# Kernel optimization log

Hardware: AMD Instinct MI355X
Metric: run time of the kernel (lower is better)

The kernel has to match this reference:

```python
import jax, jax.numpy as jnp
import numpy as np
from jax import lax

B, S, C, L = 256, 30, 62, 169   # batch, timesteps, channels(nodes), data_seg
OG, OH = 64, 64                 # out_gcn, out_gru
K1, K2, K3 = 64, 32, 14         # depthwise kernel sizes (169-63-31-13 = 62 = C)


def setup_inputs() -> dict:
    key = jax.random.key(0)
    ks = jax.random.split(key, 26)
    def n(k, shape, s=0.05):
        return jax.random.normal(k, shape, dtype=jnp.float32) * s
    inp = {
        "x": jax.random.normal(ks[0], (B, S, C, L), dtype=jnp.float32),
        "adj": jax.random.normal(ks[1], (C, C), dtype=jnp.float32),
        # depthwise-separable conv 1 (kernel 64)
        "dw1_w": n(ks[2], (C, 1, K1)), "dw1_b": n(ks[3], (C,)),
        "pw1_w": n(ks[4], (C, C, 1)), "pw1_b": n(ks[5], (C,)),
        # depthwise-separable conv 2 (kernel 32)
        "dw2_w": n(ks[6], (C, 1, K2)), "dw2_b": n(ks[7], (C,)),
        "pw2_w": n(ks[8], (C, C, 1)), "pw2_b": n(ks[9], (C,)),
        # depthwise-separable conv 3 (kernel 14)
        "dw3_w": n(ks[10], (C, 1, K3)), "dw3_b": n(ks[11], (C,)),
        "pw3_w": n(ks[12], (C, C, 1)), "pw3_b": n(ks[13], (C,)),
        # GraphConvolution(data_seg, out_gcn): support = x @ W; out = adj @ support + b
        "gcn_w": n(ks[14], (L, OG)), "gcn_b": n(ks[15], (OG,)),
        # GRU-style gate Linears (out_gcn+out_gru -> out_gru), torch layout (out, in)
        "Wr_w": n(ks[16], (OH, OG + OH)), "Wr_b": n(ks[17], (OH,)),
        "Wu_w": n(ks[18], (OH, OG + OH)), "Wu_b": n(ks[19], (OH,)),
        "Wc_w": n(ks[20], (OH, OG + OH)), "Wc_b": n(ks[21], (OH,)),
        # extra learned gate biases b_r/b_u/b_c (init zeros in torch)
        "b_r": jnp.zeros((OH,), jnp.float32),
        "b_u": jnp.zeros((OH,), jnp.float32),
        "b_c": jnp.zeros((OH,), jnp.float32),
    }
    return inp


def _dsconv(x, dw, dwb, pw, pwb):
    # x: (b, c, l); depthwise (groups=c, valid padding) then pointwise 1x1
    dn = ("NCH", "OIH", "NCH")
    y = lax.conv_general_dilated(x, dw, (1,), "VALID", dimension_numbers=dn,
                                 feature_group_count=x.shape[1]) + dwb[None, :, None]
    y = lax.conv_general_dilated(y, pw, (1,), "VALID", dimension_numbers=dn) + pwb[None, :, None]
    return y


def reference(x, adj, dw1_w, dw1_b, pw1_w, pw1_b, dw2_w, dw2_b, pw2_w, pw2_b,
              dw3_w, dw3_b, pw3_w, pw3_b, gcn_w, gcn_b,
              Wr_w, Wr_b, Wu_w, Wu_b, Wc_w, Wc_b, b_r, b_u, b_c):
    b, s, c, l = x.shape
    oh = b_r.shape[0]

    def step(h, xt):            # h: (b*c, oh), xt: (b, c, l)
        d = _dsconv(xt, dw1_w, dw1_b, pw1_w, pw1_b)
        d = _dsconv(d, dw2_w, dw2_b, pw2_w, pw2_b)
        d = _dsconv(d, dw3_w, dw3_b, pw3_w, pw3_b)      # (b, c, c)
        adj_t = jax.nn.sigmoid(d + adj)                  # adaptive adjacency
        support = jnp.einsum("bcl,lf->bcf", xt, gcn_w)
        g = jnp.einsum("bij,bjf->bif", adj_t, support) + gcn_b  # (b, c, og)
        gf = g.reshape(b * c, -1)
        cat = jnp.concatenate([gf, h], axis=-1)
        r = jax.nn.sigmoid(cat @ Wr_w.T + Wr_b + b_r)
        u = jax.nn.sigmoid(cat @ Wu_w.T + Wu_b + b_u)
        cc = jnp.tanh(jnp.concatenate([gf, r * h], axis=-1) @ Wc_w.T + Wc_b + b_c)
        h_new = u * h + (1.0 - u) * cc
        return h_new, None

    h0 = jnp.zeros((b * c, oh), x.dtype)
    xs = jnp.swapaxes(x, 0, 1)          # (s, b, c, l)
    h_last, _ = lax.scan(step, h0, xs)
    return h_last.reshape(b, c, oh)[:, -1, :]   # (b, out_gru)
```

## Files before the change

### kernel.cpp

```cpp
#include <hip/hip_runtime.h>
#include <math.h>

#define BB 256
#define SS 30
#define CC 62
#define LL 169
#define OG 64
#define OH 64
#define KK1 64
#define KK2 32
#define KK3 14
#define FLEN 108

typedef __attribute__((ext_vector_type(8))) short s16x8;
typedef __attribute__((ext_vector_type(4))) float f32x4;

__device__ __forceinline__ unsigned short f2bf(float f) {
    unsigned u = __float_as_uint(f);
    u += 0x7fffu + ((u >> 16) & 1u);
    return (unsigned short)(u >> 16);
}
__device__ __forceinline__ float bflo(unsigned v) { return __uint_as_float(v << 16); }
__device__ __forceinline__ float bfhi(unsigned v) { return __uint_as_float(v & 0xffff0000u); }

__global__ __launch_bounds__(1024) void k_setup1(
        const float* __restrict__ dw1, const float* __restrict__ dw1b,
        const float* __restrict__ pw1, const float* __restrict__ pw1b,
        const float* __restrict__ dw2, const float* __restrict__ dw2b,
        const float* __restrict__ pw2, const float* __restrict__ pw2b,
        const float* __restrict__ dw3, const float* __restrict__ dw3b,
        const float* __restrict__ pw3, const float* __restrict__ pw3b,
        const float* __restrict__ Wr, const float* __restrict__ Wrb, const float* __restrict__ br,
        const float* __restrict__ Wu, const float* __restrict__ Wub, const float* __restrict__ bu,
        const float* __restrict__ Wc, const float* __restrict__ Wcb, const float* __restrict__ bc,
        float* __restrict__ Bmg, float* __restrict__ WtAll,
        float* __restrict__ bias192, float* __restrict__ beff) {
    __shared__ float g23[CC * KK3];
    __shared__ float Am[CC * 45];
    __shared__ float by2[CC], vals[CC];
    int tid = threadIdx.x;

    for (int idx = tid; idx < OG * 192; idx += 1024) {
        int i = idx / 192, q = idx - i * 192;
        int gate = q >> 6, f = q & 63;
        const float* W = gate == 0 ? Wr : (gate == 1 ? Wu : Wc);
        WtAll[idx] = W[f * (OG + OH) + i];
    }
    if (tid < 192) {
        int gate = tid >> 6, f = tid & 63;
        const float* Wb = gate == 0 ? Wrb : (gate == 1 ? Wub : Wcb);
        const float* bb = gate == 0 ? br  : (gate == 1 ? bu  : bc);
        bias192[tid] = Wb[f] + bb[f];
    }
    for (int idx = tid; idx < CC * KK3; idx += 1024) {
        int c1 = idx / KK3, k3 = idx - c1 * KK3;
        float s = 0.f;
        for (int c2 = 0; c2 < CC; ++c2)
            s += pw3[61 * CC + c2] * pw2[c2 * CC + c1] * dw3[c2 * KK3 + k3];
        g23[idx] = s;
    }
    if (tid < CC) {
        int c1 = tid;
        float bz1 = pw1b[c1];
        for (int c0 = 0; c0 < CC; ++c0) bz1 += pw1[c1 * CC + c0] * dw1b[c0];
        float s2 = 0.f;
        for (int k = 0; k < KK2; ++k) s2 += dw2[c1 * KK2 + k];
        by2[c1] = dw2b[c1] + bz1 * s2;
    }
    __syncthreads();
    if (tid < CC) {
        int c2 = tid;
        float bz2 = pw2b[c2];
        for (int c1 = 0; c1 < CC; ++c1) bz2 += pw2[c2 * CC + c1] * by2[c1];
        float s3 = 0.f;
        for (int k = 0; k < KK3; ++k) s3 += dw3[c2 * KK3 + k];
        vals[c2] = pw3[61 * CC + c2] * (dw3b[c2] + bz2 * s3);
    }
    for (int idx = tid; idx < CC * 45; idx += 1024) {
        int c1 = idx / 45, m = idx - c1 * 45;
        int k2lo = max(0, m - (KK3 - 1));
        int k2hi = min(KK2 - 1, m);
        float s = 0.f;
        for (int k2 = k2lo; k2 <= k2hi; ++k2)
            s += dw2[c1 * KK2 + k2] * g23[c1 * KK3 + (m - k2)];
        Am[idx] = s;
    }
    __syncthreads();
    if (tid == 0) {
        float s = pw3b[61];
        for (int c2 = 0; c2 < CC; ++c2) s += vals[c2];
        *beff = s;
    }
    for (int idx = tid; idx < CC * 45; idx += 1024) {
        int c0 = idx / 45, m = idx - c0 * 45;
        float s = 0.f;
        for (int c1 = 0; c1 < CC; ++c1) s += pw1[c1 * CC + c0] * Am[c1 * 45 + m];
        Bmg[idx] = s;
    }
}

__global__ __launch_bounds__(128) void k_setupF(
        const float* __restrict__ Bmg, const float* __restrict__ dw1,
        unsigned short* __restrict__ Ftb) {
    __shared__ float Bl[45];
    int c0 = blockIdx.x;
    int o = threadIdx.x;
    if (c0 < CC && o < 45) Bl[o] = Bmg[c0 * 45 + o];
    __syncthreads();
    if (o >= 112) return;
    float s = 0.f;
    if (c0 < CC && o < FLEN) {
        int mlo = max(0, o - (KK1 - 1));
        int mhi = min(44, o);
        for (int m = mlo; m <= mhi; ++m)
            s += Bl[m] * dw1[c0 * KK1 + (o - m)];
    }
    Ftb[o * 64 + c0] = f2bf(s);
}

#define STG_ISSUE(i, s) do {                                                   \
    const float* pA = xg + 338 * cpa[i] + l0a[i];                              \
    const float* pB = pA + 169;                                                \
    asm volatile("global_load_dwordx2 %0, %1, off" : "=v"(A0[s]) : "v"(pA));   \
    asm volatile("global_load_dwordx2 %0, %1, off" : "=v"(A1[s]) : "v"(pA + 2));\
    asm volatile("global_load_dwordx2 %0, %1, off" : "=v"(B0[s]) : "v"(pB));   \
    asm volatile("global_load_dwordx2 %0, %1, off" : "=v"(B1[s]) : "v"(pB + 2));\
} while (0)

#define STG_CONSUME(i, s, VM) do {                                             \
    asm volatile("s_waitcnt vmcnt(" VM ")"                                     \
        : "+v"(A0[s]), "+v"(A1[s]), "+v"(B0[s]), "+v"(B1[s]));                 \
    unsigned d0, d1, d2, d3;                                                   \
    asm("v_cvt_pk_bf16_f32 %0, %1, %2" : "=v"(d0)                             \
        : "v"(__uint_as_float(A0[s].x)), "v"(__uint_as_float(B0[s].x)));       \
    asm("v_cvt_pk_bf16_f32 %0, %1, %2" : "=v"(d1)                             \
        : "v"(__uint_as_float(A0[s].y)), "v"(__uint_as_float(B0[s].y)));       \
    asm("v_cvt_pk_bf16_f32 %0, %1, %2" : "=v"(d2)                             \
        : "v"(__uint_as_float(A1[s].x)), "v"(__uint_as_float(B1[s].x)));       \
    asm("v_cvt_pk_bf16_f32 %0, %1, %2" : "=v"(d3)                             \
        : "v"(__uint_as_float(A1[s].y)), "v"(__uint_as_float(B1[s].y)));       \
    int l0 = l0a[i], cp = cpa[i];                                              \
    xTu[((l0 + 0) * 32 + cp) ^ (((l0 + 0) & 7) << 2)] = d0;                    \
    xTu[((l0 + 1) * 32 + cp) ^ (((l0 + 1) & 7) << 2)] = d1;                    \
    xTu[((l0 + 2) * 32 + cp) ^ (((l0 + 2) & 7) << 2)] = d2;                    \
    xTu[((l0 + 3) * 32 + cp) ^ (((l0 + 3) & 7) << 2)] = d3;                    \
} while (0)

__global__ __launch_bounds__(256, 3) void k_main(
        const float* __restrict__ x, const float* __restrict__ adj,
        const unsigned short* __restrict__ Ftb, const float* __restrict__ beff_p,
        float* __restrict__ wxb) {
    __shared__ __align__(16) unsigned short xT[176 * 64];
    __shared__ float dacc[4][64];
    __shared__ __align__(16) unsigned adjbf[32];
    int bt = blockIdx.x;
    int tid = threadIdx.x;
    int lane = tid & 63, wid = tid >> 6;
    int col = lane & 15, rb4 = lane >> 4;
    unsigned* xTu = (unsigned*)xT;
    const float* xg = x + (size_t)bt * (CC * LL);

    float be = *beff_p;
    float2 arow2 = make_float2(0.f, 0.f);
    if (tid < 31) arow2 = *(const float2*)(adj + 61 * CC + 2 * tid);
    const unsigned short* ap0 = Ftb + ((wid * 16 + col) * 64 + rb4 * 8);
    s16x8 pa0 = *(const s16x8*)ap0;
    s16x8 pa1 = *(const s16x8*)(ap0 + 32);
    int mt2c = wid + 4 < 7 ? wid + 4 : 6;
    const unsigned short* ap1 = Ftb + ((mt2c * 16 + col) * 64 + rb4 * 8);
    s16x8 pb0 = *(const s16x8*)ap1;
    s16x8 pb1 = *(const s16x8*)(ap1 + 32);
    __builtin_amdgcn_sched_barrier(0);

    uint2 A0[3], A1[3], B0[3], B1[3];
    int l0a[6], cpa[6];
    #pragma unroll
    for (int i = 0; i < 6; ++i) {
        int w = tid + i * 256; if (w > 1332) w = 1332;
        int lg = w / 31; cpa[i] = w - lg * 31;
        l0a[i] = (lg < 42) ? 4 * lg : 165;
    }
    STG_ISSUE(0, 0); STG_ISSUE(1, 1); STG_ISSUE(2, 2);
    for (int i = tid; i < 169; i += 256) xTu[(i * 32 + 31) ^ ((i & 7) << 2)] = 0;
    for (int i = tid; i < 224; i += 256) {
        int r = 169 + (i >> 5), dd = i & 31;
        xTu[(r * 32 + dd) ^ ((r & 7) << 2)] = 0;
    }
    ((float*)dacc)[tid] = 0.f;

    STG_CONSUME(0, 0, "8"); STG_ISSUE(3, 0);
    STG_CONSUME(1, 1, "8"); STG_ISSUE(4, 1);
    STG_CONSUME(2, 2, "8"); STG_ISSUE(5, 2);
    STG_CONSUME(3, 0, "8");
    STG_CONSUME(4, 1, "4");
    STG_CONSUME(5, 2, "0");
    __syncthreads();

    f32x4 zacc[5];
    #pragma unroll
    for (int d = 0; d < 5; ++d) zacc[d] = (f32x4){0.f, 0.f, 0.f, 0.f};
    int kb = rb4 * 16;
    int xr = (lane & 7) << 4;
    #pragma unroll
    for (int h = 0; h < 2; ++h) {
        int mt = wid + 4 * h;
        if (mt < 7) {
            s16x8 a0 = h == 0 ? pa0 : pb0;
            s16x8 a1 = h == 0 ? pa1 : pb1;
            #pragma unroll
            for (int d = 0; d < 5; ++d) {
                int nt = mt + d;
                int bbyte = ((nt * 16 + col) * 128 + kb) ^ xr;
                s16x8 b0 = *(const s16x8*)((const char*)xT + bbyte);
                s16x8 b1 = *(const s16x8*)((const char*)xT + (bbyte ^ 64));
                zacc[d] = __builtin_amdgcn_mfma_f32_16x16x32_bf16(a0, b0, zacc[d], 0, 0, 0);
                zacc[d] = __builtin_amdgcn_mfma_f32_16x16x32_bf16(a1, b1, zacc[d], 0, 0, 0);
            }
        }
    }
    int jc = col - rb4 * 4;
    #pragma unroll
    for (int d = 0; d < 5; ++d) {
        #pragma unroll
        for (int r = 0; r < 4; ++r) {
            int j = 16 * d + jc - r;
            if ((unsigned)j < 62u) atomicAdd(&dacc[rb4][j], zacc[d][r]);
        }
    }
    __syncthreads();

    if (tid < 32) {
        unsigned pk = 0;
        if (tid < 31) {
            int j0 = 2 * tid;
            float2 g0 = *(const float2*)(&dacc[0][j0]);
            float2 g1 = *(const float2*)(&dacc[1][j0]);
            float2 g2 = *(const float2*)(&dacc[2][j0]);
            float2 g3 = *(const float2*)(&dacc[3][j0]);
            float dv0 = (g0.x + g1.x) + (g2.x + g3.x) + be + arow2.x;
            float dv1 = (g0.y + g1.y) + (g2.y + g3.y) + be + arow2.y;
            float s0 = 1.f / (1.f + __expf(-dv0));
            float s1 = 1.f / (1.f + __expf(-dv1));
            asm("v_cvt_pk_bf16_f32 %0, %1, %2" : "=v"(pk) : "v"(s0), "v"(s1));
        }
        adjbf[tid] = pk;
    }
    __syncthreads();

    {
        s16x8 wa0 = *(const s16x8*)(adjbf + rb4 * 4);
        s16x8 wa1 = *(const s16x8*)(adjbf + 16 + rb4 * 4);
        #pragma unroll
        for (int q = 0; q < 3; ++q) {
            int nt = wid + 4 * q;
            if (nt < 11) {
                int bbyte = ((nt * 16 + col) * 128 + kb) ^ xr;
                s16x8 b0 = *(const s16x8*)((const char*)xT + bbyte);
                s16x8 b1 = *(const s16x8*)((const char*)xT + (bbyte ^ 64));
                f32x4 wacc = {0.f, 0.f, 0.f, 0.f};
                wacc = __builtin_amdgcn_mfma_f32_16x16x32_bf16(wa0, b0, wacc, 0, 0, 0);
                wacc = __builtin_amdgcn_mfma_f32_16x16x32_bf16(wa1, b1, wacc, 0, 0, 0);
                if (rb4 == 0) wxb[(size_t)bt * 176 + nt * 16 + col] = wacc[0];
            }
        }
    }
}

__global__ __launch_bounds__(256) void k_gg(
        const float* __restrict__ wxb, const float* __restrict__ gcnw,
        const float* __restrict__ gcnb, const float* __restrict__ WtAll,
        const float* __restrict__ bias192, float* __restrict__ gates) {
    __shared__ float wxl[8 * 176];
    __shared__ float Gl[8 * 64];
    int bt0 = blockIdx.x * 8;
    int tid = threadIdx.x;
    const float* src = wxb + (size_t)bt0 * 176;
    for (int i = tid; i < 8 * 176; i += 256) wxl[i] = src[i];
    __syncthreads();
    #pragma unroll
    for (int rep = 0; rep < 2; ++rep) {
        int i = rep * 256 + tid;
        int bl = i >> 6, f = i & 63;
        float s = gcnb[f];
        const float* wr = wxl + bl * 176;
        #pragma unroll 13
        for (int l = 0; l < LL; ++l) s += wr[l] * gcnw[l * OG + f];
        Gl[i] = s;
    }
    __syncthreads();
    float* gout = gates + (size_t)bt0 * 192;
    #pragma unroll
    for (int rep = 0; rep < 6; ++rep) {
        int i = rep * 256 + tid;
        int bl = i / 192, q = i - bl * 192;
        const float* gr = Gl + bl * 64;
        float s = bias192[q];
        #pragma unroll 16
        for (int k = 0; k < OG; ++k) s += gr[k] * WtAll[k * 192 + q];
        gout[i] = s;
    }
}

__global__ __launch_bounds__(256) void k_scan(
        const float* __restrict__ gates,
        const float* __restrict__ Wr, const float* __restrict__ Wu, const float* __restrict__ Wc,
        float* __restrict__ out) {
    __shared__ float hl[OH], rhl[OH];
    int b = blockIdx.x;
    int tid = threadIdx.x;
    int f = tid >> 2, q = tid & 3;
    float wr[16], wu[16], wc[16];
    #pragma unroll
    for (int i = 0; i < 16; ++i) {
        int col = OG + q * 16 + i;
        wr[i] = Wr[f * (OG + OH) + col];
        wu[i] = Wu[f * (OG + OH) + col];
        wc[i] = Wc[f * (OG + OH) + col];
    }
    float h = 0.f;
    if (tid < OH) hl[tid] = 0.f;
    __syncthreads();
    for (int t = 0; t < SS; ++t) {
        const float* gp = gates + ((size_t)b * SS + t) * 192;
        float gr = gp[f];
        float gu = gp[64 + f];
        float gc = gp[128 + f];
        float rv = 0.f, uv = 0.f;
        #pragma unroll
        for (int i = 0; i < 16; ++i) {
            float hv = hl[q * 16 + i];
            rv += wr[i] * hv;
            uv += wu[i] * hv;
        }
        rv += __shfl_xor(rv, 1); rv += __shfl_xor(rv, 2);
        uv += __shfl_xor(uv, 1); uv += __shfl_xor(uv, 2);
        float r = 1.f / (1.f + __expf(-(rv + gr)));
        float u = 1.f / (1.f + __expf(-(uv + gu)));
        if (q == 0) rhl[f] = r * h;
        __syncthreads();
        float cv = 0.f;
        #pragma unroll
        for (int i = 0; i < 16; ++i) cv += wc[i] * rhl[q * 16 + i];
        cv += __shfl_xor(cv, 1); cv += __shfl_xor(cv, 2);
        float cc = tanhf(cv + gc);
        if (q == 0) {
            h = u * h + (1.f - u) * cc;
            hl[f] = h;
        }
        __syncthreads();
    }
    if (q == 0) out[b * OH + f] = h;
}

extern "C" void kernel_launch(void* const* d_in, const int* in_sizes, int n_in,
                              void* d_out, int out_size, void* d_ws, size_t ws_size,
                              hipStream_t stream) {
    const float* x    = (const float*)d_in[0];
    const float* adj  = (const float*)d_in[1];
    const float* dw1w = (const float*)d_in[2];
    const float* dw1b = (const float*)d_in[3];
    const float* pw1w = (const float*)d_in[4];
    const float* pw1b = (const float*)d_in[5];
    const float* dw2w = (const float*)d_in[6];
    const float* dw2b = (const float*)d_in[7];
    const float* pw2w = (const float*)d_in[8];
    const float* pw2b = (const float*)d_in[9];
    const float* dw3w = (const float*)d_in[10];
    const float* dw3b = (const float*)d_in[11];
    const float* pw3w = (const float*)d_in[12];
    const float* pw3b = (const float*)d_in[13];
    const float* gcnw = (const float*)d_in[14];
    const float* gcnb = (const float*)d_in[15];
    const float* Wrw  = (const float*)d_in[16];
    const float* Wrb  = (const float*)d_in[17];
    const float* Wuw  = (const float*)d_in[18];
    const float* Wub  = (const float*)d_in[19];
    const float* Wcw  = (const float*)d_in[20];
    const float* Wcb  = (const float*)d_in[21];
    const float* br   = (const float*)d_in[22];
    const float* bu   = (const float*)d_in[23];
    const float* bc   = (const float*)d_in[24];
    float* out = (float*)d_out;

    char* ws = (char*)d_ws;
    unsigned short* Ftb = (unsigned short*)(ws + 0);
    float* WtAll        = (float*)(ws + 14336);
    float* bias192      = (float*)(ws + 63488);
    float* beff         = (float*)(ws + 64256);
    float* Bmg          = (float*)(ws + 64320);
    float* wxb          = (float*)(ws + 76800);
    float* gates        = (float*)(ws + 5483520);
    (void)ws_size; (void)in_sizes; (void)n_in; (void)out_size;

    k_setup1<<<1, 1024, 0, stream>>>(dw1w, dw1b, pw1w, pw1b, dw2w, dw2b, pw2w, pw2b,
                                     dw3w, dw3b, pw3w, pw3b,
                                     Wrw, Wrb, br, Wuw, Wub, bu, Wcw, Wcb, bc,
                                     Bmg, WtAll, bias192, beff);
    k_setupF<<<64, 128, 0, stream>>>(Bmg, dw1w, Ftb);
    k_main<<<BB * SS, 256, 0, stream>>>(x, adj, Ftb, beff, wxb);
    k_gg<<<BB * SS / 8, 256, 0, stream>>>(wxb, gcnw, gcnb, WtAll, bias192, gates);
    k_scan<<<BB, 256, 0, stream>>>(gates, Wrw, Wuw, Wcw, out);
}
```

Baseline: 280.9 us.

## Fuse GCN and gate projection into main kernel; stage x via contiguous LDS chunks

Removes the separate k_gg kernel and the wxb round trip through global memory. Each k_main block now computes the GCN output and the 192 gate pre-activations itself from an LDS copy of its wx row. The x load is also restructured: coalesced contiguous chunks of 8 channels go through a double-buffered LDS staging buffer and are then transposed into the bf16 xT layout. This adds extra LDS (about 11 KB), many block barriers in the load phase, and per-block gcnw/WtAll reads that were previously amortised over 8 rows, which may hurt occupancy under launch_bounds(256,3).

```diff
diff --git a/kernel.cpp b/kernel.cpp
--- a/kernel.cpp
+++ b/kernel.cpp
@@ -20,8 +20,6 @@
     u += 0x7fffu + ((u >> 16) & 1u);
     return (unsigned short)(u >> 16);
 }
-__device__ __forceinline__ float bflo(unsigned v) { return __uint_as_float(v << 16); }
-__device__ __forceinline__ float bfhi(unsigned v) { return __uint_as_float(v & 0xffff0000u); }
 
 __global__ __launch_bounds__(1024) void k_setup1(
         const float* __restrict__ dw1, const float* __restrict__ dw1b,
@@ -118,41 +116,68 @@
     Ftb[o * 64 + c0] = f2bf(s);
 }
 
-#define STG_ISSUE(i, s) do {                                                   \
-    const float* pA = xg + 338 * cpa[i] + l0a[i];                              \
-    const float* pB = pA + 169;                                                \
-    asm volatile("global_load_dwordx2 %0, %1, off" : "=v"(A0[s]) : "v"(pA));   \
-    asm volatile("global_load_dwordx2 %0, %1, off" : "=v"(A1[s]) : "v"(pA + 2));\
-    asm volatile("global_load_dwordx2 %0, %1, off" : "=v"(B0[s]) : "v"(pB));   \
-    asm volatile("global_load_dwordx2 %0, %1, off" : "=v"(B1[s]) : "v"(pB + 2));\
+#define CH_ISSUE(ch) do {                                                          \
+    const int nd2 = ((ch) < 7) ? 676 : 507;                                        \
+    const float* cb = xg + 1352 * (ch);                                            \
+    _Pragma("unroll")                                                              \
+    for (int j = 0; j < 3; ++j) {                                                  \
+        int pos = tid + j * 256; if (pos > nd2 - 1) pos = nd2 - 1;                 \
+        asm volatile("global_load_dwordx2 %0, %1, off"                             \
+                     : "=v"(SL[(ch) & 1][j]) : "v"(cb + 2 * pos));                 \
+    }                                                                              \
 } while (0)
 
-#define STG_CONSUME(i, s, VM) do {                                             \
-    asm volatile("s_waitcnt vmcnt(" VM ")"                                     \
-        : "+v"(A0[s]), "+v"(A1[s]), "+v"(B0[s]), "+v"(B1[s]));                 \
-    unsigned d0, d1, d2, d3;                                                   \
-    asm("v_cvt_pk_bf16_f32 %0, %1, %2" : "=v"(d0)                             \
-        : "v"(__uint_as_float(A0[s].x)), "v"(__uint_as_float(B0[s].x)));       \
-    asm("v_cvt_pk_bf16_f32 %0, %1, %2" : "=v"(d1)                             \
-        : "v"(__uint_as_float(A0[s].y)), "v"(__uint_as_float(B0[s].y)));       \
-    asm("v_cvt_pk_bf16_f32 %0, %1, %2" : "=v"(d2)                             \
-        : "v"(__uint_as_float(A1[s].x)), "v"(__uint_as_float(B1[s].x)));       \
-    asm("v_cvt_pk_bf16_f32 %0, %1, %2" : "=v"(d3)                             \
-        : "v"(__uint_as_float(A1[s].y)), "v"(__uint_as_float(B1[s].y)));       \
-    int l0 = l0a[i], cp = cpa[i];                                              \
-    xTu[((l0 + 0) * 32 + cp) ^ (((l0 + 0) & 7) << 2)] = d0;                    \
-    xTu[((l0 + 1) * 32 + cp) ^ (((l0 + 1) & 7) << 2)] = d1;                    \
-    xTu[((l0 + 2) * 32 + cp) ^ (((l0 + 2) & 7) << 2)] = d2;                    \
-    xTu[((l0 + 3) * 32 + cp) ^ (((l0 + 3) & 7) << 2)] = d3;                    \
+#define CH_CONSUME(ch, VM) do {                                                    \
+    asm volatile("s_waitcnt vmcnt(" VM ")"                                         \
+        : "+v"(SL[(ch) & 1][0]), "+v"(SL[(ch) & 1][1]), "+v"(SL[(ch) & 1][2]));    \
+    {                                                                              \
+        const int nd2 = ((ch) < 7) ? 676 : 507;                                    \
+        uint2* cb2 = (uint2*)chunkbuf[(ch) & 1];                                   \
+        _Pragma("unroll")                                                          \
+        for (int j = 0; j < 3; ++j) {                                              \
+            int pos = tid + j * 256; if (pos > nd2 - 1) pos = nd2 - 1;             \
+            cb2[pos] = SL[(ch) & 1][j];                                            \
+        }                                                                          \
+    }                                                                              \
+    asm volatile("s_waitcnt lgkmcnt(0)" ::: "memory");                             \
+    __builtin_amdgcn_sched_barrier(0);                                             \
+    __builtin_amdgcn_s_barrier();                                                  \
+    {                                                                              \
+        const int ncp = ((ch) < 7) ? 4 : 3;                                        \
+        const unsigned* cb = (const unsigned*)chunkbuf[(ch) & 1];                  \
+        int cpL = tid & 3, lb = tid >> 2;                                          \
+        _Pragma("unroll")                                                          \
+        for (int it = 0; it < 3; ++it) {                                           \
+            int l = lb + 64 * it;                                                  \
+            if (l < LL && cpL < ncp) {                                             \
+                unsigned lo = cb[(2 * cpL) * LL + l];                              \
+                unsigned hi = cb[(2 * cpL + 1) * LL + l];                          \
+                unsigned v;                                                        \
+                asm("v_cvt_pk_bf16_f32 %0, %1, %2" : "=v"(v)                       \
+                    : "v"(__uint_as_float(lo)), "v"(__uint_as_float(hi)));         \
+                int cp = (ch) * 4 + cpL;                                           \
+                xTu[(l * 32 + cp) ^ ((l & 7) << 2)] = v;                           \
+            }                                                                      \
+        }                                                                          \
+    }                                                                              \
+    asm volatile("s_waitcnt lgkmcnt(0)" ::: "memory");                             \
+    __builtin_amdgcn_sched_barrier(0);                                             \
+    __builtin_amdgcn_s_barrier();                                                  \
 } while (0)
 
 __global__ __launch_bounds__(256, 3) void k_main(
         const float* __restrict__ x, const float* __restrict__ adj,
         const unsigned short* __restrict__ Ftb, const float* __restrict__ beff_p,
-        float* __restrict__ wxb) {
+        const float* __restrict__ gcnw, const float* __restrict__ gcnb,
+        const float* __restrict__ WtAll, const float* __restrict__ bias192,
+        float* __restrict__ gates) {
     __shared__ __align__(16) unsigned short xT[176 * 64];
+    __shared__ __align__(16) char chunkbuf[2][5408];
     __shared__ float dacc[4][64];
     __shared__ __align__(16) unsigned adjbf[32];
+    __shared__ float wxl[176];
+    __shared__ float gpart[4][64];
+    __shared__ float Gl[64];
     int bt = blockIdx.x;
     int tid = threadIdx.x;
     int lane = tid & 63, wid = tid >> 6;
@@ -168,19 +193,12 @@
     s16x8 pa1 = *(const s16x8*)(ap0 + 32);
     int mt2c = wid + 4 < 7 ? wid + 4 : 6;
     const unsigned short* ap1 = Ftb + ((mt2c * 16 + col) * 64 + rb4 * 8);
-    s16x8 pb0 = *(const s16x8*)ap1;
+    s16x8 pb0 = *(const s16x8*)(ap1);
     s16x8 pb1 = *(const s16x8*)(ap1 + 32);
     __builtin_amdgcn_sched_barrier(0);
 
-    uint2 A0[3], A1[3], B0[3], B1[3];
-    int l0a[6], cpa[6];
-    #pragma unroll
-    for (int i = 0; i < 6; ++i) {
-        int w = tid + i * 256; if (w > 1332) w = 1332;
-        int lg = w / 31; cpa[i] = w - lg * 31;
-        l0a[i] = (lg < 42) ? 4 * lg : 165;
-    }
-    STG_ISSUE(0, 0); STG_ISSUE(1, 1); STG_ISSUE(2, 2);
+    uint2 SL[2][3];
+    CH_ISSUE(0); CH_ISSUE(1);
     for (int i = tid; i < 169; i += 256) xTu[(i * 32 + 31) ^ ((i & 7) << 2)] = 0;
     for (int i = tid; i < 224; i += 256) {
         int r = 169 + (i >> 5), dd = i & 31;
@@ -188,13 +206,14 @@
     }
     ((float*)dacc)[tid] = 0.f;
 
-    STG_CONSUME(0, 0, "8"); STG_ISSUE(3, 0);
-    STG_CONSUME(1, 1, "8"); STG_ISSUE(4, 1);
-    STG_CONSUME(2, 2, "8"); STG_ISSUE(5, 2);
-    STG_CONSUME(3, 0, "8");
-    STG_CONSUME(4, 1, "4");
-    STG_CONSUME(5, 2, "0");
-    __syncthreads();
+    CH_CONSUME(0, "3"); CH_ISSUE(2);
+    CH_CONSUME(1, "3"); CH_ISSUE(3);
+    CH_CONSUME(2, "3"); CH_ISSUE(4);
+    CH_CONSUME(3, "3"); CH_ISSUE(5);
+    CH_CONSUME(4, "3"); CH_ISSUE(6);
+    CH_CONSUME(5, "3"); CH_ISSUE(7);
+    CH_CONSUME(6, "3");
+    CH_CONSUME(7, "0");
 
     f32x4 zacc[5];
     #pragma unroll
@@ -260,44 +279,28 @@
                 f32x4 wacc = {0.f, 0.f, 0.f, 0.f};
                 wacc = __builtin_amdgcn_mfma_f32_16x16x32_bf16(wa0, b0, wacc, 0, 0, 0);
                 wacc = __builtin_amdgcn_mfma_f32_16x16x32_bf16(wa1, b1, wacc, 0, 0, 0);
-                if (rb4 == 0) wxb[(size_t)bt * 176 + nt * 16 + col] = wacc[0];
+                if (rb4 == 0) wxl[nt * 16 + col] = wacc[0];
             }
         }
     }
-}
-
-__global__ __launch_bounds__(256) void k_gg(
-        const float* __restrict__ wxb, const float* __restrict__ gcnw,
-        const float* __restrict__ gcnb, const float* __restrict__ WtAll,
-        const float* __restrict__ bias192, float* __restrict__ gates) {
-    __shared__ float wxl[8 * 176];
-    __shared__ float Gl[8 * 64];
-    int bt0 = blockIdx.x * 8;
-    int tid = threadIdx.x;
-    const float* src = wxb + (size_t)bt0 * 176;
-    for (int i = tid; i < 8 * 176; i += 256) wxl[i] = src[i];
-    __syncthreads();
-    #pragma unroll
-    for (int rep = 0; rep < 2; ++rep) {
-        int i = rep * 256 + tid;
-        int bl = i >> 6, f = i & 63;
-        float s = gcnb[f];
-        const float* wr = wxl + bl * 176;
-        #pragma unroll 13
-        for (int l = 0; l < LL; ++l) s += wr[l] * gcnw[l * OG + f];
-        Gl[i] = s;
-    }
-    __syncthreads();
-    float* gout = gates + (size_t)bt0 * 192;
-    #pragma unroll
-    for (int rep = 0; rep < 6; ++rep) {
-        int i = rep * 256 + tid;
-        int bl = i / 192, q = i - bl * 192;
-        const float* gr = Gl + bl * 64;
-        float s = bias192[q];
+    __syncthreads();
+
+    {
+        int f = tid & 63, lq = tid >> 6;
+        float s = 0.f;
+        for (int l = lq; l < LL; l += 4) s += wxl[l] * gcnw[l * OG + f];
+        gpart[lq][f] = s;
+    }
+    __syncthreads();
+    if (tid < OG)
+        Gl[tid] = gcnb[tid] + gpart[0][tid] + gpart[1][tid] + gpart[2][tid] + gpart[3][tid];
+    __syncthreads();
+
+    if (tid < 192) {
+        float s = bias192[tid];
         #pragma unroll 16
-        for (int k = 0; k < OG; ++k) s += gr[k] * WtAll[k * 192 + q];
-        gout[i] = s;
+        for (int k = 0; k < OG; ++k) s += Gl[k] * WtAll[k * 192 + tid];
+        gates[(size_t)bt * 192 + tid] = s;
     }
 }
 
@@ -388,8 +391,7 @@
     float* bias192      = (float*)(ws + 63488);
     float* beff         = (float*)(ws + 64256);
     float* Bmg          = (float*)(ws + 64320);
-    float* wxb          = (float*)(ws + 76800);
-    float* gates        = (float*)(ws + 5483520);
+    float* gates        = (float*)(ws + 76800);
     (void)ws_size; (void)in_sizes; (void)n_in; (void)out_size;
 
     k_setup1<<<1, 1024, 0, stream>>>(dw1w, dw1b, pw1w, pw1b, dw2w, dw2b, pw2w, pw2b,
@@ -397,7 +399,7 @@
                                      Wrw, Wrb, br, Wuw, Wub, bu, Wcw, Wcb, bc,
                                      Bmg, WtAll, bias192, beff);
     k_setupF<<<64, 128, 0, stream>>>(Bmg, dw1w, Ftb);
-    k_main<<<BB * SS, 256, 0, stream>>>(x, adj, Ftb, beff, wxb);
-    k_gg<<<BB * SS / 8, 256, 0, stream>>>(wxb, gcnw, gcnb, WtAll, bias192, gates);
+    k_main<<<BB * SS, 256, 0, stream>>>(x, adj, Ftb, beff, gcnw, gcnb,
+                                        WtAll, bias192, gates);
     k_scan<<<BB, 256, 0, stream>>>(gates, Wrw, Wuw, Wcw, out);
 }
```

Measured after the change: 341.1 us. 1.21x slower.

## Make main kernel persistent over tiles with double-buffered prefetch and fused GCN gates

Applied to the files above, without the earlier changes.

The main kernel now handles NT=10 (batch,timestep) tiles per block. The next tile's x is loaded into a second LDS buffer while the current tile's MFMA work runs. The former k_gg GCN/gate projection is fused into the per-tile loop, which removes the wxb round trip through global memory. The two setup kernels are merged into one 64-block kernel that redundantly recomputes Am per block. In exchange, the grid shrinks from 7680 to 768 blocks, LDS use doubles, and each tile now carries several extra barriers plus serial gate GEMV work that may lower occupancy.

```diff
diff --git a/kernel.cpp b/kernel.cpp
--- a/kernel.cpp
+++ b/kernel.cpp
@@ -11,6 +11,7 @@
 #define KK2 32
 #define KK3 14
 #define FLEN 108
+#define NT 10
 
 typedef __attribute__((ext_vector_type(8))) short s16x8;
 typedef __attribute__((ext_vector_type(4))) float f32x4;
@@ -20,10 +21,8 @@
     u += 0x7fffu + ((u >> 16) & 1u);
     return (unsigned short)(u >> 16);
 }
-__device__ __forceinline__ float bflo(unsigned v) { return __uint_as_float(v << 16); }
-__device__ __forceinline__ float bfhi(unsigned v) { return __uint_as_float(v & 0xffff0000u); }
-
-__global__ __launch_bounds__(1024) void k_setup1(
+
+__global__ __launch_bounds__(128) void k_setupAll(
         const float* __restrict__ dw1, const float* __restrict__ dw1b,
         const float* __restrict__ pw1, const float* __restrict__ pw1b,
         const float* __restrict__ dw2, const float* __restrict__ dw2b,
@@ -33,42 +32,44 @@
         const float* __restrict__ Wr, const float* __restrict__ Wrb, const float* __restrict__ br,
         const float* __restrict__ Wu, const float* __restrict__ Wub, const float* __restrict__ bu,
         const float* __restrict__ Wc, const float* __restrict__ Wcb, const float* __restrict__ bc,
-        float* __restrict__ Bmg, float* __restrict__ WtAll,
+        unsigned short* __restrict__ Ftb, float* __restrict__ WtAll,
         float* __restrict__ bias192, float* __restrict__ beff) {
     __shared__ float g23[CC * KK3];
     __shared__ float Am[CC * 45];
+    __shared__ float Bl[45];
     __shared__ float by2[CC], vals[CC];
-    int tid = threadIdx.x;
-
-    for (int idx = tid; idx < OG * 192; idx += 1024) {
-        int i = idx / 192, q = idx - i * 192;
+    int c0 = blockIdx.x, tid = threadIdx.x;
+
+    for (int q = tid; q < 192; q += 128) {
         int gate = q >> 6, f = q & 63;
         const float* W = gate == 0 ? Wr : (gate == 1 ? Wu : Wc);
-        WtAll[idx] = W[f * (OG + OH) + i];
-    }
-    if (tid < 192) {
-        int gate = tid >> 6, f = tid & 63;
-        const float* Wb = gate == 0 ? Wrb : (gate == 1 ? Wub : Wcb);
-        const float* bb = gate == 0 ? br  : (gate == 1 ? bu  : bc);
-        bias192[tid] = Wb[f] + bb[f];
-    }
-    for (int idx = tid; idx < CC * KK3; idx += 1024) {
+        WtAll[c0 * 192 + q] = W[f * (OG + OH) + c0];
+    }
+    if (c0 == 0) {
+        for (int q = tid; q < 192; q += 128) {
+            int gate = q >> 6, f = q & 63;
+            const float* Wb = gate == 0 ? Wrb : (gate == 1 ? Wub : Wcb);
+            const float* bb = gate == 0 ? br  : (gate == 1 ? bu  : bc);
+            bias192[q] = Wb[f] + bb[f];
+        }
+    }
+    if (c0 == 63 && tid < CC) {
+        int c1 = tid;
+        float bz1 = pw1b[c1];
+        for (int cc = 0; cc < CC; ++cc) bz1 += pw1[c1 * CC + cc] * dw1b[cc];
+        float s2 = 0.f;
+        for (int k = 0; k < KK2; ++k) s2 += dw2[c1 * KK2 + k];
+        by2[c1] = dw2b[c1] + bz1 * s2;
+    }
+    for (int idx = tid; idx < CC * KK3; idx += 128) {
         int c1 = idx / KK3, k3 = idx - c1 * KK3;
         float s = 0.f;
         for (int c2 = 0; c2 < CC; ++c2)
             s += pw3[61 * CC + c2] * pw2[c2 * CC + c1] * dw3[c2 * KK3 + k3];
         g23[idx] = s;
     }
-    if (tid < CC) {
-        int c1 = tid;
-        float bz1 = pw1b[c1];
-        for (int c0 = 0; c0 < CC; ++c0) bz1 += pw1[c1 * CC + c0] * dw1b[c0];
-        float s2 = 0.f;
-        for (int k = 0; k < KK2; ++k) s2 += dw2[c1 * KK2 + k];
-        by2[c1] = dw2b[c1] + bz1 * s2;
-    }
     __syncthreads();
-    if (tid < CC) {
+    if (c0 == 63 && tid < CC) {
         int c2 = tid;
         float bz2 = pw2b[c2];
         for (int c1 = 0; c1 < CC; ++c1) bz2 += pw2[c2 * CC + c1] * by2[c1];
@@ -76,7 +77,7 @@
         for (int k = 0; k < KK3; ++k) s3 += dw3[c2 * KK3 + k];
         vals[c2] = pw3[61 * CC + c2] * (dw3b[c2] + bz2 * s3);
     }
-    for (int idx = tid; idx < CC * 45; idx += 1024) {
+    for (int idx = tid; idx < CC * 45; idx += 128) {
         int c1 = idx / 45, m = idx - c1 * 45;
         int k2lo = max(0, m - (KK3 - 1));
         int k2hi = min(KK2 - 1, m);
@@ -86,40 +87,32 @@
         Am[idx] = s;
     }
     __syncthreads();
-    if (tid == 0) {
+    if (c0 == 63 && tid == 0) {
         float s = pw3b[61];
         for (int c2 = 0; c2 < CC; ++c2) s += vals[c2];
         *beff = s;
     }
-    for (int idx = tid; idx < CC * 45; idx += 1024) {
-        int c0 = idx / 45, m = idx - c0 * 45;
+    if (tid < 45 && c0 < CC) {
         float s = 0.f;
-        for (int c1 = 0; c1 < CC; ++c1) s += pw1[c1 * CC + c0] * Am[c1 * 45 + m];
-        Bmg[idx] = s;
+        for (int c1 = 0; c1 < CC; ++c1) s += pw1[c1 * CC + c0] * Am[c1 * 45 + tid];
+        Bl[tid] = s;
+    }
+    __syncthreads();
+    if (tid < 112) {
+        int o = tid;
+        float s = 0.f;
+        if (c0 < CC && o < FLEN) {
+            int mlo = max(0, o - (KK1 - 1));
+            int mhi = min(44, o);
+            for (int m = mlo; m <= mhi; ++m)
+                s += Bl[m] * dw1[c0 * KK1 + (o - m)];
+        }
+        Ftb[o * 64 + c0] = f2bf(s);
     }
 }
 
-__global__ __launch_bounds__(128) void k_setupF(
-        const float* __restrict__ Bmg, const float* __restrict__ dw1,
-        unsigned short* __restrict__ Ftb) {
-    __shared__ float Bl[45];
-    int c0 = blockIdx.x;
-    int o = threadIdx.x;
-    if (c0 < CC && o < 45) Bl[o] = Bmg[c0 * 45 + o];
-    __syncthreads();
-    if (o >= 112) return;
-    float s = 0.f;
-    if (c0 < CC && o < FLEN) {
-        int mlo = max(0, o - (KK1 - 1));
-        int mhi = min(44, o);
-        for (int m = mlo; m <= mhi; ++m)
-            s += Bl[m] * dw1[c0 * KK1 + (o - m)];
-    }
-    Ftb[o * 64 + c0] = f2bf(s);
-}
-
-#define STG_ISSUE(i, s) do {                                                   \
-    const float* pA = xg + 338 * cpa[i] + l0a[i];                              \
+#define SISSUE(tp, i, s) do {                                                  \
+    const float* pA = (tp) + 338 * cpa[i] + l0a[i];                            \
     const float* pB = pA + 169;                                                \
     asm volatile("global_load_dwordx2 %0, %1, off" : "=v"(A0[s]) : "v"(pA));   \
     asm volatile("global_load_dwordx2 %0, %1, off" : "=v"(A1[s]) : "v"(pA + 2));\
@@ -127,7 +120,7 @@
     asm volatile("global_load_dwordx2 %0, %1, off" : "=v"(B1[s]) : "v"(pB + 2));\
 } while (0)
 
-#define STG_CONSUME(i, s, VM) do {                                             \
+#define SCONSUME(i, s, VM, XW) do {                                            \
     asm volatile("s_waitcnt vmcnt(" VM ")"                                     \
         : "+v"(A0[s]), "+v"(A1[s]), "+v"(B0[s]), "+v"(B1[s]));                 \
     unsigned d0, d1, d2, d3;                                                   \
@@ -140,25 +133,29 @@
     asm("v_cvt_pk_bf16_f32 %0, %1, %2" : "=v"(d3)                             \
         : "v"(__uint_as_float(A1[s].y)), "v"(__uint_as_float(B1[s].y)));       \
     int l0 = l0a[i], cp = cpa[i];                                              \
-    xTu[((l0 + 0) * 32 + cp) ^ (((l0 + 0) & 7) << 2)] = d0;                    \
-    xTu[((l0 + 1) * 32 + cp) ^ (((l0 + 1) & 7) << 2)] = d1;                    \
-    xTu[((l0 + 2) * 32 + cp) ^ (((l0 + 2) & 7) << 2)] = d2;                    \
-    xTu[((l0 + 3) * 32 + cp) ^ (((l0 + 3) & 7) << 2)] = d3;                    \
+    (XW)[((l0 + 0) * 32 + cp) ^ (((l0 + 0) & 7) << 2)] = d0;                   \
+    (XW)[((l0 + 1) * 32 + cp) ^ (((l0 + 1) & 7) << 2)] = d1;                   \
+    (XW)[((l0 + 2) * 32 + cp) ^ (((l0 + 2) & 7) << 2)] = d2;                   \
+    (XW)[((l0 + 3) * 32 + cp) ^ (((l0 + 3) & 7) << 2)] = d3;                   \
 } while (0)
 
 __global__ __launch_bounds__(256, 3) void k_main(
         const float* __restrict__ x, const float* __restrict__ adj,
         const unsigned short* __restrict__ Ftb, const float* __restrict__ beff_p,
-        float* __restrict__ wxb) {
-    __shared__ __align__(16) unsigned short xT[176 * 64];
+        const float* __restrict__ gcnw, const float* __restrict__ gcnb,
+        const float* __restrict__ WtAll, const float* __restrict__ bias192,
+        float* __restrict__ gates) {
+    __shared__ __align__(16) unsigned short xT[2][176 * 64];
     __shared__ float dacc[4][64];
     __shared__ __align__(16) unsigned adjbf[32];
-    int bt = blockIdx.x;
+    __shared__ float wxl[176];
+    __shared__ float gpart[4][64];
+    __shared__ float Gl[64];
     int tid = threadIdx.x;
     int lane = tid & 63, wid = tid >> 6;
     int col = lane & 15, rb4 = lane >> 4;
     unsigned* xTu = (unsigned*)xT;
-    const float* xg = x + (size_t)bt * (CC * LL);
+    int btBase = blockIdx.x * NT;
 
     float be = *beff_p;
     float2 arow2 = make_float2(0.f, 0.f);
@@ -168,7 +165,7 @@
     s16x8 pa1 = *(const s16x8*)(ap0 + 32);
     int mt2c = wid + 4 < 7 ? wid + 4 : 6;
     const unsigned short* ap1 = Ftb + ((mt2c * 16 + col) * 64 + rb4 * 8);
-    s16x8 pb0 = *(const s16x8*)ap1;
+    s16x8 pb0 = *(const s16x8*)(ap1);
     s16x8 pb1 = *(const s16x8*)(ap1 + 32);
     __builtin_amdgcn_sched_barrier(0);
 
@@ -180,124 +177,133 @@
         int lg = w / 31; cpa[i] = w - lg * 31;
         l0a[i] = (lg < 42) ? 4 * lg : 165;
     }
-    STG_ISSUE(0, 0); STG_ISSUE(1, 1); STG_ISSUE(2, 2);
-    for (int i = tid; i < 169; i += 256) xTu[(i * 32 + 31) ^ ((i & 7) << 2)] = 0;
-    for (int i = tid; i < 224; i += 256) {
-        int r = 169 + (i >> 5), dd = i & 31;
-        xTu[(r * 32 + dd) ^ ((r & 7) << 2)] = 0;
-    }
-    ((float*)dacc)[tid] = 0.f;
-
-    STG_CONSUME(0, 0, "8"); STG_ISSUE(3, 0);
-    STG_CONSUME(1, 1, "8"); STG_ISSUE(4, 1);
-    STG_CONSUME(2, 2, "8"); STG_ISSUE(5, 2);
-    STG_CONSUME(3, 0, "8");
-    STG_CONSUME(4, 1, "4");
-    STG_CONSUME(5, 2, "0");
-    __syncthreads();
-
-    f32x4 zacc[5];
-    #pragma unroll
-    for (int d = 0; d < 5; ++d) zacc[d] = (f32x4){0.f, 0.f, 0.f, 0.f};
     int kb = rb4 * 16;
     int xr = (lane & 7) << 4;
-    #pragma unroll
-    for (int h = 0; h < 2; ++h) {
-        int mt = wid + 4 * h;
-        if (mt < 7) {
-            s16x8 a0 = h == 0 ? pa0 : pb0;
-            s16x8 a1 = h == 0 ? pa1 : pb1;
+    int jc = col - rb4 * 4;
+
+    {
+        const float* tp0 = x + (size_t)btBase * (CC * LL);
+        SISSUE(tp0, 0, 0); SISSUE(tp0, 1, 1); SISSUE(tp0, 2, 2);
+        for (int b = 0; b < 2; ++b) {
+            unsigned* XW = xTu + b * 5632;
+            for (int i = tid; i < 169; i += 256) XW[(i * 32 + 31) ^ ((i & 7) << 2)] = 0;
+            for (int i = tid; i < 224; i += 256) {
+                int r = 169 + (i >> 5), dd = i & 31;
+                XW[(r * 32 + dd) ^ ((r & 7) << 2)] = 0;
+            }
+        }
+        ((float*)dacc)[tid] = 0.f;
+        unsigned* XW0 = xTu;
+        SCONSUME(0, 0, "8", XW0); SISSUE(tp0, 3, 0);
+        SCONSUME(1, 1, "8", XW0); SISSUE(tp0, 4, 1);
+        SCONSUME(2, 2, "8", XW0); SISSUE(tp0, 5, 2);
+        SCONSUME(3, 0, "8", XW0);
+        SCONSUME(4, 1, "4", XW0);
+        SCONSUME(5, 2, "0", XW0);
+        __syncthreads();
+    }
+
+    for (int t = 0; t < NT; ++t) {
+        int cur = t & 1;
+        const char* xTb = (const char*)xT + cur * 22528;
+        unsigned* XWn = xTu + (cur ^ 1) * 5632;
+        bool more = (t + 1 < NT);
+        const float* tpn = x + (size_t)(btBase + (more ? t + 1 : t)) * (CC * LL);
+        if (more) { SISSUE(tpn, 0, 0); SISSUE(tpn, 1, 1); SISSUE(tpn, 2, 2); }
+
+        f32x4 zacc[5];
+        #pragma unroll
+        for (int d = 0; d < 5; ++d) zacc[d] = (f32x4){0.f, 0.f, 0.f, 0.f};
+        #pragma unroll
+        for (int h = 0; h < 2; ++h) {
+            int mt = wid + 4 * h;
+            if (mt < 7) {
+                s16x8 a0 = h == 0 ? pa0 : pb0;
+                s16x8 a1 = h == 0 ? pa1 : pb1;
+                #pragma unroll
+                for (int d = 0; d < 5; ++d) {
+                    int nt = mt + d;
+                    int bbyte = ((nt * 16 + col) * 128 + kb) ^ xr;
+                    s16x8 b0 = *(const s16x8*)(xTb + bbyte);
+                    s16x8 b1 = *(const s16x8*)(xTb + (bbyte ^ 64));
+                    zacc[d] = __builtin_amdgcn_mfma_f32_16x16x32_bf16(a0, b0, zacc[d], 0, 0, 0);
+                    zacc[d] = __builtin_amdgcn_mfma_f32_16x16x32_bf16(a1, b1, zacc[d], 0, 0, 0);
+                }
+            }
+        }
+        if (more) { SCONSUME(0, 0, "8", XWn); SISSUE(tpn, 3, 0); }
+        #pragma unroll
+        for (int d = 0; d < 5; ++d) {
             #pragma unroll
-            for (int d = 0; d < 5; ++d) {
-                int nt = mt + d;
-                int bbyte = ((nt * 16 + col) * 128 + kb) ^ xr;
-                s16x8 b0 = *(const s16x8*)((const char*)xT + bbyte);
-                s16x8 b1 = *(const s16x8*)((const char*)xT + (bbyte ^ 64));
-                zacc[d] = __builtin_amdgcn_mfma_f32_16x16x32_bf16(a0, b0, zacc[d], 0, 0, 0);
-                zacc[d] = __builtin_amdgcn_mfma_f32_16x16x32_bf16(a1, b1, zacc[d], 0, 0, 0);
+            for (int r = 0; r < 4; ++r) {
+                int j = 16 * d + jc - r;
+                if ((unsigned)j < 62u) atomicAdd(&dacc[rb4][j], zacc[d][r]);
             }
         }
-    }
-    int jc = col - rb4 * 4;
-    #pragma unroll
-    for (int d = 0; d < 5; ++d) {
-        #pragma unroll
-        for (int r = 0; r < 4; ++r) {
-            int j = 16 * d + jc - r;
-            if ((unsigned)j < 62u) atomicAdd(&dacc[rb4][j], zacc[d][r]);
-        }
-    }
-    __syncthreads();
-
-    if (tid < 32) {
-        unsigned pk = 0;
-        if (tid < 31) {
-            int j0 = 2 * tid;
-            float2 g0 = *(const float2*)(&dacc[0][j0]);
-            float2 g1 = *(const float2*)(&dacc[1][j0]);
-            float2 g2 = *(const float2*)(&dacc[2][j0]);
-            float2 g3 = *(const float2*)(&dacc[3][j0]);
-            float dv0 = (g0.x + g1.x) + (g2.x + g3.x) + be + arow2.x;
-            float dv1 = (g0.y + g1.y) + (g2.y + g3.y) + be + arow2.y;
-            float s0 = 1.f / (1.f + __expf(-dv0));
-            float s1 = 1.f / (1.f + __expf(-dv1));
-            asm("v_cvt_pk_bf16_f32 %0, %1, %2" : "=v"(pk) : "v"(s0), "v"(s1));
-        }
-        adjbf[tid] = pk;
-    }
-    __syncthreads();
-
-    {
-        s16x8 wa0 = *(const s16x8*)(adjbf + rb4 * 4);
-        s16x8 wa1 = *(const s16x8*)(adjbf + 16 + rb4 * 4);
-        #pragma unroll
-        for (int q = 0; q < 3; ++q) {
-            int nt = wid + 4 * q;
-            if (nt < 11) {
-                int bbyte = ((nt * 16 + col) * 128 + kb) ^ xr;
-                s16x8 b0 = *(const s16x8*)((const char*)xT + bbyte);
-                s16x8 b1 = *(const s16x8*)((const char*)xT + (bbyte ^ 64));
-                f32x4 wacc = {0.f, 0.f, 0.f, 0.f};
-                wacc = __builtin_amdgcn_mfma_f32_16x16x32_bf16(wa0, b0, wacc, 0, 0, 0);
-                wacc = __builtin_amdgcn_mfma_f32_16x16x32_bf16(wa1, b1, wacc, 0, 0, 0);
-                if (rb4 == 0) wxb[(size_t)bt * 176 + nt * 16 + col] = wacc[0];
+        if (more) { SCONSUME(1, 1, "8", XWn); SISSUE(tpn, 4, 1); }
+        __syncthreads();
+
+        if (more) { SCONSUME(2, 2, "8", XWn); SISSUE(tpn, 5, 2); }
+        if (tid < 32) {
+            unsigned pk = 0;
+            if (tid < 31) {
+                int j0 = 2 * tid;
+                float2 g0 = *(const float2*)(&dacc[0][j0]);
+                float2 g1 = *(const float2*)(&dacc[1][j0]);
+                float2 g2 = *(const float2*)(&dacc[2][j0]);
+                float2 g3 = *(const float2*)(&dacc[3][j0]);
+                float dv0 = (g0.x + g1.x) + (g2.x + g3.x) + be + arow2.x;
+                float dv1 = (g0.y + g1.y) + (g2.y + g3.y) + be + arow2.y;
+                float s0 = 1.f / (1.f + __expf(-dv0));
+                float s1 = 1.f / (1.f + __expf(-dv1));
+                asm("v_cvt_pk_bf16_f32 %0, %1, %2" : "=v"(pk) : "v"(s0), "v"(s1));
             }
-        }
-    }
-}
-
-__global__ __launch_bounds__(256) void k_gg(
-        const float* __restrict__ wxb, const float* __restrict__ gcnw,
-        const float* __restrict__ gcnb, const float* __restrict__ WtAll,
-        const float* __restrict__ bias192, float* __restrict__ gates) {
-    __shared__ float wxl[8 * 176];
-    __shared__ float Gl[8 * 64];
-    int bt0 = blockIdx.x * 8;
-    int tid = threadIdx.x;
-    const float* src = wxb + (size_t)bt0 * 176;
-    for (int i = tid; i < 8 * 176; i += 256) wxl[i] = src[i];
-    __syncthreads();
-    #pragma unroll
-    for (int rep = 0; rep < 2; ++rep) {
-        int i = rep * 256 + tid;
-        int bl = i >> 6, f = i & 63;
-        float s = gcnb[f];
-        const float* wr = wxl + bl * 176;
-        #pragma unroll 13
-        for (int l = 0; l < LL; ++l) s += wr[l] * gcnw[l * OG + f];
-        Gl[i] = s;
-    }
-    __syncthreads();
-    float* gout = gates + (size_t)bt0 * 192;
-    #pragma unroll
-    for (int rep = 0; rep < 6; ++rep) {
-        int i = rep * 256 + tid;
-        int bl = i / 192, q = i - bl * 192;
-        const float* gr = Gl + bl * 64;
-        float s = bias192[q];
-        #pragma unroll 16
-        for (int k = 0; k < OG; ++k) s += gr[k] * WtAll[k * 192 + q];
-        gout[i] = s;
+            adjbf[tid] = pk;
+        }
+        __syncthreads();
+
+        if (more) { SCONSUME(3, 0, "8", XWn); }
+        {
+            s16x8 wa0 = *(const s16x8*)(adjbf + rb4 * 4);
+            s16x8 wa1 = *(const s16x8*)(adjbf + 16 + rb4 * 4);
+            #pragma unroll
+            for (int q = 0; q < 3; ++q) {
+                int nt = wid + 4 * q;
+                if (nt < 11) {
+                    int bbyte = ((nt * 16 + col) * 128 + kb) ^ xr;
+                    s16x8 b0 = *(const s16x8*)(xTb + bbyte);
+                    s16x8 b1 = *(const s16x8*)(xTb + (bbyte ^ 64));
+                    f32x4 wacc = {0.f, 0.f, 0.f, 0.f};
+                    wacc = __builtin_amdgcn_mfma_f32_16x16x32_bf16(wa0, b0, wacc, 0, 0, 0);
+                    wacc = __builtin_amdgcn_mfma_f32_16x16x32_bf16(wa1, b1, wacc, 0, 0, 0);
+                    if (rb4 == 0) wxl[nt * 16 + col] = wacc[0];
+                }
+            }
+        }
+        ((float*)dacc)[tid] = 0.f;
+        __syncthreads();
+
+        if (more) { SCONSUME(4, 1, "4", XWn); }
+        {
+            int f = tid & 63, lq = tid >> 6;
+            float s = 0.f;
+            for (int l = lq; l < LL; l += 4) s += wxl[l] * gcnw[l * OG + f];
+            gpart[lq][f] = s;
+        }
+        __syncthreads();
+
+        if (more) { SCONSUME(5, 2, "0", XWn); }
+        if (tid < OG)
+            Gl[tid] = gcnb[tid] + gpart[0][tid] + gpart[1][tid] + gpart[2][tid] + gpart[3][tid];
+        __syncthreads();
+
+        if (tid < 192) {
+            float s = bias192[tid];
+            #pragma unroll 16
+            for (int k = 0; k < OG; ++k) s += Gl[k] * WtAll[k * 192 + tid];
+            gates[(size_t)(btBase + t) * 192 + tid] = s;
+        }
+        __syncthreads();
     }
 }
 
@@ -387,17 +393,14 @@
     float* WtAll        = (float*)(ws + 14336);
     float* bias192      = (float*)(ws + 63488);
     float* beff         = (float*)(ws + 64256);
-    float* Bmg          = (float*)(ws + 64320);
-    float* wxb          = (float*)(ws + 76800);
-    float* gates        = (float*)(ws + 5483520);
+    float* gates        = (float*)(ws + 76800);
     (void)ws_size; (void)in_sizes; (void)n_in; (void)out_size;
 
-    k_setup1<<<1, 1024, 0, stream>>>(dw1w, dw1b, pw1w, pw1b, dw2w, dw2b, pw2w, pw2b,
-                                     dw3w, dw3b, pw3w, pw3b,
-                                     Wrw, Wrb, br, Wuw, Wub, bu, Wcw, Wcb, bc,
-                                     Bmg, WtAll, bias192, beff);
-    k_setupF<<<64, 128, 0, stream>>>(Bmg, dw1w, Ftb);
-    k_main<<<BB * SS, 256, 0, stream>>>(x, adj, Ftb, beff, wxb);
-    k_gg<<<BB * SS / 8, 256, 0, stream>>>(wxb, gcnw, gcnb, WtAll, bias192, gates);
+    k_setupAll<<<64, 128, 0, stream>>>(dw1w, dw1b, pw1w, pw1b, dw2w, dw2b, pw2w, pw2b,
+                                       dw3w, dw3b, pw3w, pw3b,
+                                       Wrw, Wrb, br, Wuw, Wub, bu, Wcw, Wcb, bc,
+                                       Ftb, WtAll, bias192, beff);
+    k_main<<<BB * SS / NT, 256, 0, stream>>>(x, adj, Ftb, beff, gcnw, gcnb,
+                                             WtAll, bias192, gates);
     k_scan<<<BB, 256, 0, stream>>>(gates, Wrw, Wuw, Wcw, out);
 }
```

After: 421.2 us. 49.9% more time.
